# Kernel tuning notes

Hardware: AMD Instinct MI355X
Metric: run time of the kernel (lower is better)

Reference implementation:

```python
import jax, jax.numpy as jnp
import numpy as np

S = 7
B = 2
C = 80
N = 8192
LAMBD_COORD = 5.0
LAMBD_NOOBJ = 0.5


def setup_inputs() -> dict:
    key = jax.random.key(0)
    k1, k2, k3 = jax.random.split(key, 3)
    prediction = jax.random.uniform(k1, (N, S, S, B * 5 + C), dtype=jnp.float32)
    target = jax.random.uniform(k2, (N, S, S, 5 + C), dtype=jnp.float32)
    conf = (jax.random.uniform(k3, (N, S, S)) > 0.7).astype(jnp.float32)
    target = target.at[..., 4].set(conf)
    return {"prediction": prediction, "target": target}


def _rel2abs(box):
    # box: (N,S,S,>=4) with (xcr_rcell, ycr_rcell, wr, hr); returns corner coords (image-relative)
    x, y, w, h = box[..., 0], box[..., 1], box[..., 2], box[..., 3]
    jj = jnp.arange(S, dtype=box.dtype)[None, None, :]   # cell_j -> x axis
    ii = jnp.arange(S, dtype=box.dtype)[None, :, None]   # cell_i -> y axis
    xc = (x + jj) / S
    yc = (y + ii) / S
    return xc - w / 2, yc - h / 2, xc + w / 2, yc + h / 2


def _iou(a, b):
    ax1, ay1, ax2, ay2 = a
    bx1, by1, bx2, by2 = b
    iw = jnp.clip(jnp.minimum(ax2, bx2) - jnp.maximum(ax1, bx1), 0.0)
    ih = jnp.clip(jnp.minimum(ay2, by2) - jnp.maximum(ay1, by1), 0.0)
    inter = iw * ih
    area_a = (ax2 - ax1) * (ay2 - ay1)
    area_b = (bx2 - bx1) * (by2 - by1)
    return inter / (area_a + area_b - inter + 1e-6)


def reference(prediction, target):
    tgt_abs = _rel2abs(target[..., :5])
    iou0 = _iou(tgt_abs, _rel2abs(prediction[..., 0:5]))
    iou1 = _iou(tgt_abs, _rel2abs(prediction[..., 5:10]))
    # faithful to source: mask True (iou0 > iou1) selects offset idx = 5 (second box)
    sel_mask = (iou0 > iou1)[..., None]                              # (N,S,S,1)
    box_sel = jnp.where(sel_mask, prediction[..., 5:10], prediction[..., 0:5])
    xy_hat = box_sel[..., 0:2]
    wh_hat = box_sel[..., 2:4]

    xy = target[..., 0:2]
    wh = target[..., 2:4]
    # faithful to source: pred_c uses box_k after the loop, i.e. 4 + 5*(B-1)
    pred_c = prediction[..., 4 + 5 * (B - 1)]
    true_c = target[..., 4]

    obj = (true_c != 0)                  # contributions kept where object present
    objf = obj.astype(prediction.dtype)
    noobjf = 1.0 - objf

    # xy loss
    loss_xy_cell = objf * jnp.sum((xy - xy_hat) ** 2, axis=-1)

    # wh loss with sqrt-safe masking (masked entries contribute 0, matching masked_fill)
    obj_e = obj[..., None]
    wh_safe = jnp.where(obj_e, wh, 1.0)
    wh_hat_safe = jnp.where(obj_e, jnp.maximum(wh_hat, 0.0), 1.0)
    loss_wh_cell = objf * jnp.sum((jnp.sqrt(wh_safe) - jnp.sqrt(wh_hat_safe)) ** 2, axis=-1)

    # confidence losses
    conf_se = (true_c - pred_c) ** 2
    loss_conf_obj_cell = objf * conf_se
    loss_conf_noobj_cell = noobjf * conf_se

    # class loss
    pred_class = prediction[..., 5 * B:]
    true_class = target[..., 5:]
    loss_class_cell = objf * jnp.sum((true_class - pred_class) ** 2, axis=-1)

    bs = prediction.shape[0]
    loss_xy = jnp.sum(loss_xy_cell) / bs
    loss_wh = jnp.sum(loss_wh_cell) / bs
    loss_conf_obj = jnp.sum(loss_conf_obj_cell) / bs
    loss_conf_noobj = jnp.sum(loss_conf_noobj_cell) / bs
    loss_class = jnp.sum(loss_class_cell) / bs

    # faithful to source: weighted sum divided by BATCH_SIZE once more
    loss = (LAMBD_COORD * loss_xy + LAMBD_COORD * loss_wh + loss_conf_obj
            + LAMBD_NOOBJ * loss_conf_noobj + loss_class) / bs
    return loss, loss_xy, loss_wh, loss_conf_obj, loss_conf_noobj, loss_class
```

## Files before the change

### kernel.cpp

```cpp
#include <hip/hip_runtime.h>


#define NCELLS (8192 * 49)
#define CPT 4
#define TPW 16
#define WPB 4
#define CELLS_PER_BLOCK (CPT * TPW * WPB)
#define NBLOCKS (NCELLS / CELLS_PER_BLOCK)
#define TFL (CPT * 85)
#define PFL (CPT * 90)
#define BUF_FL (TFL + PFL)

constexpr float BSF = 8192.0f;

__device__ __forceinline__ void g2lds16(const float* g, float* s) {
    __builtin_amdgcn_global_load_lds(
        (const __attribute__((address_space(1))) void*)g,
        (__attribute__((address_space(3))) void*)s,
        16, 0, 0);
}

__device__ __forceinline__ void rel2abs(float x, float y, float w, float h,
                                        float fi, float fj,
                                        float& x1, float& y1, float& x2, float& y2) {
    float xc = (x + fj) / 7.0f;
    float yc = (y + fi) / 7.0f;
    float hw = w * 0.5f, hh = h * 0.5f;
    x1 = xc - hw; y1 = yc - hh; x2 = xc + hw; y2 = yc + hh;
}

__device__ __forceinline__ float iou_abs(float ax1, float ay1, float ax2, float ay2,
                                         float bx1, float by1, float bx2, float by2) {
    float iw = fminf(ax2, bx2) - fmaxf(ax1, bx1); iw = fmaxf(iw, 0.0f);
    float ih = fminf(ay2, by2) - fmaxf(ay1, by1); ih = fmaxf(ih, 0.0f);
    float inter  = iw * ih;
    float area_a = (ax2 - ax1) * (ay2 - ay1);
    float area_b = (bx2 - bx1) * (by2 - by1);
    return inter / (area_a + area_b - inter + 1e-6f);
}

__device__ __forceinline__ void stage_tile(const float* __restrict__ tg,
                                           const float* __restrict__ pg,
                                           float* wbuf, int lane) {
    g2lds16(tg + 4 * lane, wbuf + 4 * lane);
    if (lane < 21) g2lds16(tg + 256 + 4 * lane, wbuf + 256 + 4 * lane);
    g2lds16(pg + 4 * lane, wbuf + TFL + 4 * lane);
    if (lane < 26) g2lds16(pg + 256 + 4 * lane, wbuf + TFL + 256 + 4 * lane);
}

__global__ __launch_bounds__(256, 7) void yolo_main(const float* __restrict__ pred,
                                                    const float* __restrict__ tgt,
                                                    float* __restrict__ acc,
                                                    int nrep, int sstride) {
    __shared__ __align__(16) float lds[WPB][2][BUF_FL];
    __shared__ float smr[WPB * 5];

    const int tid  = threadIdx.x;
    const int lane = tid & 63;
    const int wid  = tid >> 6;

    const int wave_id = blockIdx.x * WPB + wid;
    const int tile0   = wave_id * TPW;

    const float* tg0 = tgt  + (size_t)tile0 * TFL;
    const float* pg0 = pred + (size_t)tile0 * PFL;

    float a_xy = 0.f, a_wh = 0.f, a_co = 0.f, a_cn = 0.f, a_cl = 0.f;

    const int cell = lane >> 4;
    const int part = lane & 15;
    const int c0   = 5 * part;

    float* cur = &lds[wid][0][0];
    float* nxt = &lds[wid][1][0];

    stage_tile(tg0, pg0, cur, lane);

    for (int k = 0; k < TPW; ++k) {
        if (k + 1 < TPW) {
            asm volatile("s_waitcnt lgkmcnt(0)" ::: "memory");
            stage_tile(tg0 + (size_t)(k + 1) * TFL,
                       pg0 + (size_t)(k + 1) * PFL, nxt, lane);
            asm volatile("s_waitcnt vmcnt(4)" ::: "memory");
        } else {
            asm volatile("s_waitcnt vmcnt(0)" ::: "memory");
        }

        const float* tb = cur + 85 * cell;
        const float* pb = cur + TFL + 90 * cell;

        const float objf = (tb[4] != 0.0f) ? 1.0f : 0.0f;

        float s = 0.f;
        #pragma unroll
        for (int c = 0; c < 5; ++c) {
            float d = tb[5 + c0 + c] - pb[10 + c0 + c];
            s = fmaf(d, d, s);
        }
        a_cl += objf * s;

        if (part == 0) {
            float tx = tb[0], ty = tb[1], tw = tb[2], th = tb[3], tc = tb[4];
            float p0x = pb[0], p0y = pb[1], p0w = pb[2], p0h = pb[3];
            float p1x = pb[5], p1y = pb[6], p1w = pb[7], p1h = pb[8];
            float pc  = pb[9];

            int gcell = (tile0 + k) * CPT + cell;
            int sij   = gcell % 49;
            float fi  = (float)(sij / 7);
            float fj  = (float)(sij % 7);

            float t1, t2, t3, t4, a1, a2, a3, a4, b1, b2, b3, b4;
            rel2abs(tx,  ty,  tw,  th,  fi, fj, t1, t2, t3, t4);
            rel2abs(p0x, p0y, p0w, p0h, fi, fj, a1, a2, a3, a4);
            rel2abs(p1x, p1y, p1w, p1h, fi, fj, b1, b2, b3, b4);

            float iou0 = iou_abs(t1, t2, t3, t4, a1, a2, a3, a4);
            float iou1 = iou_abs(t1, t2, t3, t4, b1, b2, b3, b4);

            bool sel = iou0 > iou1;
            float xh = sel ? p1x : p0x;
            float yh = sel ? p1y : p0y;
            float wh = sel ? p1w : p0w;
            float hh = sel ? p1h : p0h;

            float dx = tx - xh, dy = ty - yh;
            a_xy += objf * (dx * dx + dy * dy);

            float sw = sqrtf(tw) - sqrtf(fmaxf(wh, 0.0f));
            float sh = sqrtf(th) - sqrtf(fmaxf(hh, 0.0f));
            a_wh += objf * (sw * sw + sh * sh);

            float ce = tc - pc; ce *= ce;
            a_co += objf * ce;
            a_cn += (1.0f - objf) * ce;
        }

        float* tmp = cur; cur = nxt; nxt = tmp;
    }

    #pragma unroll
    for (int off = 32; off; off >>= 1) {
        a_xy += __shfl_down(a_xy, off, 64);
        a_wh += __shfl_down(a_wh, off, 64);
        a_co += __shfl_down(a_co, off, 64);
        a_cn += __shfl_down(a_cn, off, 64);
        a_cl += __shfl_down(a_cl, off, 64);
    }
    if (lane == 0) {
        smr[wid * 5 + 0] = a_xy; smr[wid * 5 + 1] = a_wh; smr[wid * 5 + 2] = a_co;
        smr[wid * 5 + 3] = a_cn; smr[wid * 5 + 4] = a_cl;
    }
    __syncthreads();
    if (tid == 0) {
        float s0 = 0.f, s1 = 0.f, s2 = 0.f, s3 = 0.f, s4 = 0.f;
        #pragma unroll
        for (int w = 0; w < 4; ++w) {
            s0 += smr[w * 5 + 0]; s1 += smr[w * 5 + 1]; s2 += smr[w * 5 + 2];
            s3 += smr[w * 5 + 3]; s4 += smr[w * 5 + 4];
        }
        const int rep = (int)(blockIdx.x & (unsigned)(nrep - 1));
        float* a0 = acc + (size_t)rep * 5 * sstride;
        atomicAdd(&a0[0 * sstride], s0);
        atomicAdd(&a0[1 * sstride], s1);
        atomicAdd(&a0[2 * sstride], s2);
        atomicAdd(&a0[3 * sstride], s3);
        atomicAdd(&a0[4 * sstride], s4);
    }
}

__global__ void yolo_finalize(const float* __restrict__ acc, float* __restrict__ out,
                              int nrep, int sstride) {
    if (threadIdx.x == 0 && blockIdx.x == 0) {
        float s[5] = {0.f, 0.f, 0.f, 0.f, 0.f};
        for (int r = 0; r < nrep; ++r)
            for (int k = 0; k < 5; ++k)
                s[k] += acc[((size_t)r * 5 + k) * sstride];
        float lxy = s[0] / BSF;
        float lwh = s[1] / BSF;
        float lco = s[2] / BSF;
        float lcn = s[3] / BSF;
        float lcl = s[4] / BSF;
        out[0] = (5.0f * lxy + 5.0f * lwh + lco + 0.5f * lcn + lcl) / BSF;
        out[1] = lxy;
        out[2] = lwh;
        out[3] = lco;
        out[4] = lcn;
        out[5] = lcl;
    }
}

extern "C" void kernel_launch(void* const* d_in, const int* in_sizes, int n_in,
                              void* d_out, int out_size, void* d_ws, size_t ws_size,
                              hipStream_t stream) {
    const float* pred = (const float*)d_in[0];
    const float* tgt  = (const float*)d_in[1];
    float* out = (float*)d_out;
    float* acc = (float*)d_ws;

    int nrep, sstride; size_t zbytes;
    if (ws_size >= 8 * 5 * 32 * sizeof(float)) { nrep = 8; sstride = 32; zbytes = 8 * 5 * 32 * sizeof(float); }
    else                                       { nrep = 1; sstride = 1;  zbytes = 5 * sizeof(float); }

    hipMemsetAsync(acc, 0, zbytes, stream);

    yolo_main<<<NBLOCKS, 256, 0, stream>>>(pred, tgt, acc, nrep, sstride);
    yolo_finalize<<<1, 64, 0, stream>>>(acc, out, nrep, sstride);
}
```

Measured before the change: 320.0 us.

## Replace LDS double-buffered staging with direct global loads, 8 lanes per cell

Drops the per-wave global_load_lds double-buffer pipeline and has each group of 8 lanes read one cell's target and prediction rows directly from global memory, using float2 loads for prediction. Each block now covers 256 cells over 8 iterations, and the launch-bounds occupancy hint drops from 7 to 6. This removes LDS traffic, the manual waitcnt synchronization and the LDS footprint. In exchange, target loads are unaligned scalar accesses with a stride of 85 floats, so coalescing is poorer and latency hiding depends on occupancy and the unroll by 2 rather than explicit prefetch.

```diff
diff --git a/kernel.cpp b/kernel.cpp
--- a/kernel.cpp
+++ b/kernel.cpp
@@ -2,23 +2,11 @@
 
 
 #define NCELLS (8192 * 49)
-#define CPT 4
-#define TPW 16
-#define WPB 4
-#define CELLS_PER_BLOCK (CPT * TPW * WPB)
+#define NITER 8
+#define CELLS_PER_BLOCK 256
 #define NBLOCKS (NCELLS / CELLS_PER_BLOCK)
-#define TFL (CPT * 85)
-#define PFL (CPT * 90)
-#define BUF_FL (TFL + PFL)
 
 constexpr float BSF = 8192.0f;
-
-__device__ __forceinline__ void g2lds16(const float* g, float* s) {
-    __builtin_amdgcn_global_load_lds(
-        (const __attribute__((address_space(1))) void*)g,
-        (__attribute__((address_space(3))) void*)s,
-        16, 0, 0);
-}
 
 __device__ __forceinline__ void rel2abs(float x, float y, float w, float h,
                                         float fi, float fj,
@@ -39,104 +27,86 @@
     return inter / (area_a + area_b - inter + 1e-6f);
 }
 
-__device__ __forceinline__ void stage_tile(const float* __restrict__ tg,
-                                           const float* __restrict__ pg,
-                                           float* wbuf, int lane) {
-    g2lds16(tg + 4 * lane, wbuf + 4 * lane);
-    if (lane < 21) g2lds16(tg + 256 + 4 * lane, wbuf + 256 + 4 * lane);
-    g2lds16(pg + 4 * lane, wbuf + TFL + 4 * lane);
-    if (lane < 26) g2lds16(pg + 256 + 4 * lane, wbuf + TFL + 256 + 4 * lane);
-}
-
-__global__ __launch_bounds__(256, 7) void yolo_main(const float* __restrict__ pred,
+__global__ __launch_bounds__(256, 6) void yolo_main(const float* __restrict__ pred,
                                                     const float* __restrict__ tgt,
                                                     float* __restrict__ acc,
                                                     int nrep, int sstride) {
-    __shared__ __align__(16) float lds[WPB][2][BUF_FL];
-    __shared__ float smr[WPB * 5];
+    __shared__ float smr[4 * 5];
 
     const int tid  = threadIdx.x;
     const int lane = tid & 63;
     const int wid  = tid >> 6;
-
-    const int wave_id = blockIdx.x * WPB + wid;
-    const int tile0   = wave_id * TPW;
-
-    const float* tg0 = tgt  + (size_t)tile0 * TFL;
-    const float* pg0 = pred + (size_t)tile0 * PFL;
+    const int c8   = lane >> 3;
+    const int p    = lane & 7;
 
     float a_xy = 0.f, a_wh = 0.f, a_co = 0.f, a_cn = 0.f, a_cl = 0.f;
 
-    const int cell = lane >> 4;
-    const int part = lane & 15;
-    const int c0   = 5 * part;
+    const int cell0 = blockIdx.x * CELLS_PER_BLOCK + wid * 8 + c8;
 
-    float* cur = &lds[wid][0][0];
-    float* nxt = &lds[wid][1][0];
+    #pragma unroll 2
+    for (int k = 0; k < NITER; ++k) {
+        const int cell = cell0 + k * 32;
+        const float* tb = tgt  + (size_t)cell * 85;
+        const float* pb = pred + (size_t)cell * 90;
 
-    stage_tile(tg0, pg0, cur, lane);
+        const float tc   = tb[4];
+        const float objf = (tc != 0.0f) ? 1.0f : 0.0f;
 
-    for (int k = 0; k < TPW; ++k) {
-        if (k + 1 < TPW) {
-            asm volatile("s_waitcnt lgkmcnt(0)" ::: "memory");
-            stage_tile(tg0 + (size_t)(k + 1) * TFL,
-                       pg0 + (size_t)(k + 1) * PFL, nxt, lane);
-            asm volatile("s_waitcnt vmcnt(4)" ::: "memory");
-        } else {
-            asm volatile("s_waitcnt vmcnt(0)" ::: "memory");
-        }
-
-        const float* tb = cur + 85 * cell;
-        const float* pb = cur + TFL + 90 * cell;
-
-        const float objf = (tb[4] != 0.0f) ? 1.0f : 0.0f;
-
+        const float* tcl = tb + 5  + 10 * p;
+        const float* pcl = pb + 10 + 10 * p;
         float s = 0.f;
         #pragma unroll
-        for (int c = 0; c < 5; ++c) {
-            float d = tb[5 + c0 + c] - pb[10 + c0 + c];
-            s = fmaf(d, d, s);
+        for (int m = 0; m < 5; ++m) {
+            const float2 pv = *reinterpret_cast<const float2*>(pcl + 2 * m);
+            const float t0 = tcl[2 * m];
+            const float t1 = tcl[2 * m + 1];
+            const float d0 = t0 - pv.x;
+            const float d1 = t1 - pv.y;
+            s = fmaf(d0, d0, s);
+            s = fmaf(d1, d1, s);
         }
         a_cl += objf * s;
 
-        if (part == 0) {
-            float tx = tb[0], ty = tb[1], tw = tb[2], th = tb[3], tc = tb[4];
-            float p0x = pb[0], p0y = pb[1], p0w = pb[2], p0h = pb[3];
-            float p1x = pb[5], p1y = pb[6], p1w = pb[7], p1h = pb[8];
-            float pc  = pb[9];
+        if (p == 0) {
+            const float tx = tb[0], ty = tb[1], tw = tb[2], th = tb[3];
+            const float2 q01 = *reinterpret_cast<const float2*>(pb + 0);
+            const float2 q23 = *reinterpret_cast<const float2*>(pb + 2);
+            const float2 q45 = *reinterpret_cast<const float2*>(pb + 4);
+            const float2 q67 = *reinterpret_cast<const float2*>(pb + 6);
+            const float2 q89 = *reinterpret_cast<const float2*>(pb + 8);
+            const float p0x = q01.x, p0y = q01.y, p0w = q23.x, p0h = q23.y;
+            const float p1x = q45.y, p1y = q67.x, p1w = q67.y, p1h = q89.x;
+            const float pc  = q89.y;
 
-            int gcell = (tile0 + k) * CPT + cell;
-            int sij   = gcell % 49;
-            float fi  = (float)(sij / 7);
-            float fj  = (float)(sij % 7);
+            const int sij = cell % 49;
+            const float fi = (float)(sij / 7);
+            const float fj = (float)(sij % 7);
 
-            float t1, t2, t3, t4, a1, a2, a3, a4, b1, b2, b3, b4;
-            rel2abs(tx,  ty,  tw,  th,  fi, fj, t1, t2, t3, t4);
+            float t1_, t2_, t3_, t4_, a1, a2, a3, a4, b1, b2, b3, b4;
+            rel2abs(tx,  ty,  tw,  th,  fi, fj, t1_, t2_, t3_, t4_);
             rel2abs(p0x, p0y, p0w, p0h, fi, fj, a1, a2, a3, a4);
             rel2abs(p1x, p1y, p1w, p1h, fi, fj, b1, b2, b3, b4);
 
-            float iou0 = iou_abs(t1, t2, t3, t4, a1, a2, a3, a4);
-            float iou1 = iou_abs(t1, t2, t3, t4, b1, b2, b3, b4);
+            const float iou0 = iou_abs(t1_, t2_, t3_, t4_, a1, a2, a3, a4);
+            const float iou1 = iou_abs(t1_, t2_, t3_, t4_, b1, b2, b3, b4);
 
-            bool sel = iou0 > iou1;
-            float xh = sel ? p1x : p0x;
-            float yh = sel ? p1y : p0y;
-            float wh = sel ? p1w : p0w;
-            float hh = sel ? p1h : p0h;
+            const bool sel = iou0 > iou1;
+            const float xh = sel ? p1x : p0x;
+            const float yh = sel ? p1y : p0y;
+            const float wh = sel ? p1w : p0w;
+            const float hh = sel ? p1h : p0h;
 
-            float dx = tx - xh, dy = ty - yh;
+            const float dx = tx - xh, dy = ty - yh;
             a_xy += objf * (dx * dx + dy * dy);
 
-            float sw = sqrtf(tw) - sqrtf(fmaxf(wh, 0.0f));
-            float sh = sqrtf(th) - sqrtf(fmaxf(hh, 0.0f));
+            const float sw = sqrtf(tw) - sqrtf(fmaxf(wh, 0.0f));
+            const float sh = sqrtf(th) - sqrtf(fmaxf(hh, 0.0f));
             a_wh += objf * (sw * sw + sh * sh);
 
             float ce = tc - pc; ce *= ce;
             a_co += objf * ce;
             a_cn += (1.0f - objf) * ce;
         }
-
-        float* tmp = cur; cur = nxt; nxt = tmp;
     }
 
     #pragma unroll
```

Result: no change. 314.2 us (-1.8%).
